# Optimization experiments

Measured on AMD Instinct MI355X. Metric: run time of the kernel, lower is better.

## Reference

```python
import jax, jax.numpy as jnp
import numpy as np

D_MODEL = 1024
N_HEADS = 16
CHUNK = 64
EPS = 1e-6


def elu_plus_1(x):
    return jax.nn.elu(x) + 1.0


def setup_inputs() -> dict:
    key = jax.random.key(0)
    kx, kq, kk, kv, ko = jax.random.split(key, 5)
    B, T = 4, 4096
    # xavier_uniform for square (D, D) weights: limit = sqrt(6/(D+D))
    lim = float(np.sqrt(6.0 / (D_MODEL + D_MODEL)))
    mk = lambda k: jax.random.uniform(k, (D_MODEL, D_MODEL), jnp.float32, -lim, lim)
    return {
        "x": jax.random.normal(kx, (B, T, D_MODEL), jnp.float32),
        "W_q": mk(kq),
        "W_k": mk(kk),
        "W_v": mk(kv),
        "W_o": mk(ko),
    }


def reference(x, W_q, W_k, W_v, W_o):
    B, T, D = x.shape
    H = N_HEADS
    dk = D // H
    dv = dk
    C = CHUNK
    N = T // C  # T chosen divisible by chunk size (no padding needed)

    q = (x @ W_q.T).reshape(B, T, H, dk)
    k = (x @ W_k.T).reshape(B, T, H, dk)
    v = (x @ W_v.T).reshape(B, T, H, dv)

    phi_q = elu_plus_1(q).reshape(B, N, C, H, dk)
    phi_k = elu_plus_1(k).reshape(B, N, C, H, dk)
    vc = v.reshape(B, N, C, H, dv)

    # Per-chunk key-value outer products and key sums, then exclusive prefix
    # sums over chunks give the carried state S and normalizer z at each
    # chunk's start (same math as the sequential chunk loop).
    KV = jnp.einsum('bnchk,bnchv->bnhkv', phi_k, vc)      # (B,N,H,dk,dv)
    Ksum = phi_k.sum(axis=2)                               # (B,N,C->sum,H,dk) -> (B,N,H,dk)
    KV_cum = jnp.cumsum(KV, axis=1)
    Ksum_cum = jnp.cumsum(Ksum, axis=1)
    S_prefix = jnp.concatenate([jnp.zeros_like(KV_cum[:, :1]), KV_cum[:, :-1]], axis=1)
    z_prefix = jnp.concatenate([jnp.zeros_like(Ksum_cum[:, :1]), Ksum_cum[:, :-1]], axis=1)

    # Inter-chunk contribution from carried state
    inter = jnp.einsum('bnchk,bnhkv->bnchv', phi_q, S_prefix)   # (B,N,C,H,dv)
    z_inter = jnp.einsum('bnchk,bnhk->bnch', phi_q, z_prefix)   # (B,N,C,H)

    # Intra-chunk causal attention
    mask = jnp.tril(jnp.ones((C, C), dtype=x.dtype))
    attn = jnp.einsum('bnihk,bnjhk->bnhij', phi_q, phi_k) * mask  # (B,N,H,C,C)
    intra = jnp.einsum('bnhij,bnjhv->bnihv', attn, vc)            # (B,N,C,H,dv)
    z_intra = attn.sum(axis=-1).transpose(0, 1, 3, 2)             # (B,N,C,H)

    denom = jnp.clip((z_inter + z_intra)[..., None], 1e-6, None)
    y = (inter + intra) / denom                                   # (B,N,C,H,dv)
    y = y.reshape(B, T, H * dv)
    return y @ W_o.T
```

## Files before the change

kernel.cpp:

```cpp
#include <hip/hip_runtime.h>


typedef unsigned short u16;
typedef float  f32x4 __attribute__((ext_vector_type(4)));
typedef short  b16x8 __attribute__((ext_vector_type(8)));
typedef u16    u16x4 __attribute__((ext_vector_type(4)));
typedef u16    u16x8 __attribute__((ext_vector_type(8)));

#define DEVINL __device__ __forceinline__

DEVINL u16 f2b(float f) {
  unsigned u = __float_as_uint(f);
  return (u16)((u + 0x7fffu + ((u >> 16) & 1u)) >> 16);
}
DEVINL float b2f(u16 s) { return __uint_as_float(((unsigned)s) << 16); }

DEVINL f32x4 mfma16(b16x8 a, b16x8 b, f32x4 c) {
  return __builtin_amdgcn_mfma_f32_16x16x32_bf16(a, b, c, 0, 0, 0);
}

DEVINL float phi_elu1(float v) { return v > 0.f ? v + 1.f : __expf(v); }

__global__ void cvt_kernel(const float* __restrict__ in, u16* __restrict__ out, int n8) {
  int stride = gridDim.x * blockDim.x;
  for (int i = blockIdx.x * blockDim.x + threadIdx.x; i < n8; i += stride) {
    const float* p = in + (size_t)i * 8;
    f32x4 a = *(const f32x4*)p;
    f32x4 b = *(const f32x4*)(p + 4);
    u16x8 o;
    o[0] = f2b(a[0]); o[1] = f2b(a[1]); o[2] = f2b(a[2]); o[3] = f2b(a[3]);
    o[4] = f2b(b[0]); o[5] = f2b(b[1]); o[6] = f2b(b[2]); o[7] = f2b(b[3]);
    *(u16x8*)(out + (size_t)i * 8) = o;
  }
}

__global__ void cvt4_kernel(const float* __restrict__ p0, const float* __restrict__ p1,
                            const float* __restrict__ p2, const float* __restrict__ p3,
                            u16* __restrict__ o0, u16* __restrict__ o1,
                            u16* __restrict__ o2, u16* __restrict__ o3) {
  const float* in; u16* out;
  switch (blockIdx.y) {
    case 0: in = p0; out = o0; break;
    case 1: in = p1; out = o1; break;
    case 2: in = p2; out = o2; break;
    default: in = p3; out = o3; break;
  }
  int i = blockIdx.x * blockDim.x + threadIdx.x;
  const float* p = in + (size_t)i * 8;
  f32x4 a = *(const f32x4*)p;
  f32x4 b = *(const f32x4*)(p + 4);
  u16x8 o;
  o[0] = f2b(a[0]); o[1] = f2b(a[1]); o[2] = f2b(a[2]); o[3] = f2b(a[3]);
  o[4] = f2b(b[0]); o[5] = f2b(b[1]); o[6] = f2b(b[2]); o[7] = f2b(b[3]);
  *(u16x8*)(out + (size_t)i * 8) = o;
}

#define GEMM_SETUP                                                              \
  __shared__ char lds[131072];                                                  \
  const int tid = threadIdx.x, wid = tid >> 6, l = tid & 63;                    \
  const int l15 = l & 15, lg = l >> 4;                                          \
  const int wr = wid >> 2, wc = wid & 3;                                        \
  const int ntn = N >> 8;                                                       \
  const int nwg = gridDim.x, bid = blockIdx.x;                                  \
  const int cpx = nwg >> 3;                                                     \
  const int sb = (bid & 7) * cpx + (bid >> 3);                                  \
  const int tm = sb / ntn, tn = sb - tm * ntn;                                  \
  const int colX0 = (lg * 16) ^ ((l15 & 7) << 4);                               \
  const int colX1 = (64 + lg * 16) ^ ((l15 & 7) << 4);                          \
  char* ldsA = lds + wr * 16384 + l15 * 128;                                    \
  char* ldsB = lds + 32768 + (wc >> 1) * 16384 + ((wc & 1) * 64 + l15) * 128;   \
  const int srow = tid >> 3;                                                    \
  const int scol = ((((tid & 7) * 16) ^ ((srow & 7) << 4)) >> 1);               \
  const u16* sA = A + (size_t)(tm * 256 + srow) * 1024 + scol;                  \
  const u16* sB = B + (size_t)(tn * 256 + srow) * 1024 + scol;                  \
  char* ldsStage = lds + wid * 1024;

#define STAGE(tt, h)                                                            \
  do {                                                                          \
    const u16* s_ = ((h) < 2 ? sA : sB) + (size_t)(((h) & 1) * 128) * 1024 +    \
                    (size_t)(tt) * 64;                                          \
    char* d_ = ldsStage + (((tt) & 1) << 16) + ((h) < 2 ? 0 : 32768) +          \
               (((h) & 1) << 14);                                               \
    __builtin_amdgcn_global_load_lds(                                           \
        (const __attribute__((address_space(1))) void*)(s_),                    \
        (__attribute__((address_space(3))) void*)(d_), 16, 0, 0);               \
    __builtin_amdgcn_global_load_lds(                                           \
        (const __attribute__((address_space(1))) void*)(s_ + 64 * 1024),        \
        (__attribute__((address_space(3))) void*)(d_ + 8192), 16, 0, 0);        \
  } while (0)

#define BAR_SB()                                                                \
  do {                                                                          \
    __builtin_amdgcn_s_barrier();                                               \
    __builtin_amdgcn_sched_barrier(0);                                          \
  } while (0)

#define GEMM_EPILOGUE                                                           \
  _Pragma("unroll") for (int fm = 0; fm < 8; ++fm)                              \
    _Pragma("unroll") for (int fn = 0; fn < 4; ++fn)                            \
      _Pragma("unroll") for (int r = 0; r < 4; ++r) {                           \
        size_t grow = (size_t)tm * 256 + wr * 128 + fm * 16 + lg * 4 + r;       \
        size_t gcol = (size_t)tn * 256 + wc * 64 + fn * 16 + l15;               \
        float v = acc[fm][fn][r];                                               \
        if (PHI) v = phi_elu1(v);                                               \
        OT* p = C + grow * (size_t)N + gcol;                                    \
        if constexpr (sizeof(OT) == 2) *p = (OT)f2b(v);                         \
        else                           *p = (OT)v;                              \
      }

template <bool PHI, typename OT>
__global__ __launch_bounds__(512, 2) void gemm256f(const u16* __restrict__ A,
                                                   const u16* __restrict__ B,
                                                   OT* __restrict__ C, int M, int N) {
  GEMM_SETUP

  f32x4 acc[8][4];
#pragma unroll
  for (int i = 0; i < 8; i++)
#pragma unroll
    for (int j = 0; j < 4; j++) acc[i][j] = f32x4{0.f, 0.f, 0.f, 0.f};

  STAGE(0, 0); STAGE(0, 1); STAGE(0, 2); STAGE(0, 3);
  STAGE(1, 2); STAGE(1, 3);
  asm volatile("s_waitcnt vmcnt(4)" ::: "memory");

  b16x8 a0[4], a1[4], b0[4], b1[4];
  for (int t = 0; t < 16; ++t) {
    const int cb = (t & 1) << 16;
    BAR_SB();
#pragma unroll
    for (int fm = 0; fm < 4; fm++) a0[fm] = *(const b16x8*)(ldsA + cb + fm * 2048 + colX0);
#pragma unroll
    for (int fn = 0; fn < 4; fn++) b0[fn] = *(const b16x8*)(ldsB + cb + fn * 2048 + colX0);
    if (t < 15) STAGE(t + 1, 0);
    __builtin_amdgcn_s_setprio(1);
#pragma unroll
    for (int fm = 0; fm < 4; fm++)
#pragma unroll
      for (int fn = 0; fn < 4; fn++) acc[fm][fn] = mfma16(a0[fm], b0[fn], acc[fm][fn]);
    __builtin_amdgcn_s_setprio(0);
    BAR_SB();
#pragma unroll
    for (int fm = 0; fm < 4; fm++) a1[fm] = *(const b16x8*)(ldsA + cb + (4 + fm) * 2048 + colX0);
#pragma unroll
    for (int fn = 0; fn < 4; fn++) b1[fn] = *(const b16x8*)(ldsB + cb + fn * 2048 + colX1);
    if (t < 15) STAGE(t + 1, 1);
    __builtin_amdgcn_s_setprio(1);
#pragma unroll
    for (int fm = 0; fm < 4; fm++)
#pragma unroll
      for (int fn = 0; fn < 4; fn++) acc[4 + fm][fn] = mfma16(a1[fm], b0[fn], acc[4 + fm][fn]);
    __builtin_amdgcn_s_setprio(0);
    BAR_SB();
#pragma unroll
    for (int fm = 0; fm < 4; fm++) a0[fm] = *(const b16x8*)(ldsA + cb + fm * 2048 + colX1);
    if (t < 14) STAGE(t + 2, 2);
    __builtin_amdgcn_s_setprio(1);
#pragma unroll
    for (int fm = 0; fm < 4; fm++)
#pragma unroll
      for (int fn = 0; fn < 4; fn++) acc[fm][fn] = mfma16(a0[fm], b1[fn], acc[fm][fn]);
    __builtin_amdgcn_s_setprio(0);
    BAR_SB();
#pragma unroll
    for (int fm = 0; fm < 4; fm++) a1[fm] = *(const b16x8*)(ldsA + cb + (4 + fm) * 2048 + colX1);
    if (t < 14) STAGE(t + 2, 3);
    __builtin_amdgcn_s_setprio(1);
#pragma unroll
    for (int fm = 0; fm < 4; fm++)
#pragma unroll
      for (int fn = 0; fn < 4; fn++) acc[4 + fm][fn] = mfma16(a1[fm], b1[fn], acc[4 + fm][fn]);
    __builtin_amdgcn_s_setprio(0);
    if (t < 14) asm volatile("s_waitcnt vmcnt(4)" ::: "memory");
    else        asm volatile("s_waitcnt vmcnt(0)" ::: "memory");
  }

  GEMM_EPILOGUE
}

template <bool PHI, typename OT>
__global__ __launch_bounds__(512, 2) void gemm256g(const u16* __restrict__ A,
                                                   const u16* __restrict__ B,
                                                   OT* __restrict__ C, int M, int N) {
  GEMM_SETUP

  f32x4 acc[8][4];
#pragma unroll
  for (int i = 0; i < 8; i++)
#pragma unroll
    for (int j = 0; j < 4; j++) acc[i][j] = f32x4{0.f, 0.f, 0.f, 0.f};

  STAGE(0, 0); STAGE(0, 1); STAGE(0, 2); STAGE(0, 3);
  STAGE(1, 2); STAGE(1, 3);
  asm volatile("s_waitcnt vmcnt(4)" ::: "memory");

  b16x8 a0[4], a1[4], b0[4], b1[4];
  for (int t = 0; t < 16; ++t) {
    const int cb = (t & 1) << 16;
    BAR_SB();
#pragma unroll
    for (int fm = 0; fm < 4; fm++) {
      a0[fm] = *(const b16x8*)(ldsA + cb + fm * 2048 + colX0);
      a1[fm] = *(const b16x8*)(ldsA + cb + (4 + fm) * 2048 + colX0);
    }
#pragma unroll
    for (int fn = 0; fn < 4; fn++) b0[fn] = *(const b16x8*)(ldsB + cb + fn * 2048 + colX0);
    if (t < 15) { STAGE(t + 1, 0); STAGE(t + 1, 1); }
    __builtin_amdgcn_s_setprio(1);
#pragma unroll
    for (int fm = 0; fm < 4; fm++)
#pragma unroll
      for (int fn = 0; fn < 4; fn++) acc[fm][fn] = mfma16(a0[fm], b0[fn], acc[fm][fn]);
#pragma unroll
    for (int fm = 0; fm < 4; fm++)
#pragma unroll
      for (int fn = 0; fn < 4; fn++) acc[4 + fm][fn] = mfma16(a1[fm], b0[fn], acc[4 + fm][fn]);
    __builtin_amdgcn_s_setprio(0);
    BAR_SB();
#pragma unroll
    for (int fm = 0; fm < 4; fm++) {
      a0[fm] = *(const b16x8*)(ldsA + cb + fm * 2048 + colX1);
      a1[fm] = *(const b16x8*)(ldsA + cb + (4 + fm) * 2048 + colX1);
    }
#pragma unroll
    for (int fn = 0; fn < 4; fn++) b1[fn] = *(const b16x8*)(ldsB + cb + fn * 2048 + colX1);
    if (t < 14) { STAGE(t + 2, 2); STAGE(t + 2, 3); }
    __builtin_amdgcn_s_setprio(1);
#pragma unroll
    for (int fm = 0; fm < 4; fm++)
#pragma unroll
      for (int fn = 0; fn < 4; fn++) acc[fm][fn] = mfma16(a0[fm], b1[fn], acc[fm][fn]);
#pragma unroll
    for (int fm = 0; fm < 4; fm++)
#pragma unroll
      for (int fn = 0; fn < 4; fn++) acc[4 + fm][fn] = mfma16(a1[fm], b1[fn], acc[4 + fm][fn]);
    __builtin_amdgcn_s_setprio(0);
    if (t < 14) asm volatile("s_waitcnt vmcnt(4)" ::: "memory");
    else        asm volatile("s_waitcnt vmcnt(0)" ::: "memory");
  }

  GEMM_EPILOGUE
}

__global__ __launch_bounds__(256) void transpose64(const u16* __restrict__ in,
                                                   u16* __restrict__ out) {
  __shared__ u16 tile[64][68];
  const int t = threadIdx.x;
  const int tr = blockIdx.x, tc = blockIdx.y;
#pragma unroll
  for (int i = 0; i < 4; i++) {
    int idx = i * 256 + t, r = idx >> 4, c4 = idx & 15;
    u16x4 v = *(const u16x4*)(in + (size_t)(tr * 64 + r) * 1024 + tc * 64 + c4 * 4);
    *(u16x4*)&tile[r][c4 * 4] = v;
  }
  __syncthreads();
#pragma unroll
  for (int i = 0; i < 4; i++) {
    int idx = i * 256 + t, oc = idx >> 4, r4 = idx & 15;
    u16x4 v;
    v[0] = tile[r4 * 4 + 0][oc]; v[1] = tile[r4 * 4 + 1][oc];
    v[2] = tile[r4 * 4 + 2][oc]; v[3] = tile[r4 * 4 + 3][oc];
    *(u16x4*)(out + (size_t)(tc * 64 + oc) * 16384 + tr * 64 + r4 * 4) = v;
  }
}

__global__ __launch_bounds__(256, 2) void kv_kernel(const u16* __restrict__ kT,
                                                    const u16* __restrict__ vT,
                                                    u16* __restrict__ KVT,
                                                    float* __restrict__ Ksum) {
  const int tid = threadIdx.x, wid = tid >> 6, l = tid & 63, l15 = l & 15, lg = l >> 4;
  const int bid = blockIdx.x, hg = bid & 3, bn = bid >> 2, n = bn & 63, b = bn >> 6;
  const int h = hg * 4 + wid;
  const size_t cb = (size_t)b * 4096 + n * 64 + lg * 8;

  b16x8 af[4][2], bf[4][2];
#pragma unroll
  for (int fm = 0; fm < 4; fm++)
#pragma unroll
    for (int ks = 0; ks < 2; ks++)
      af[fm][ks] = *(const b16x8*)(vT + (size_t)(h * 64 + fm * 16 + l15) * 16384 + cb + ks * 32);
#pragma unroll
  for (int fn = 0; fn < 4; fn++)
#pragma unroll
    for (int ks = 0; ks < 2; ks++)
      bf[fn][ks] = *(const b16x8*)(kT + (size_t)(h * 64 + fn * 16 + l15) * 16384 + cb + ks * 32);

  f32x4 acc[4][4];
#pragma unroll
  for (int i = 0; i < 4; i++)
#pragma unroll
    for (int j = 0; j < 4; j++) acc[i][j] = f32x4{0.f, 0.f, 0.f, 0.f};
#pragma unroll
  for (int ks = 0; ks < 2; ks++)
#pragma unroll
    for (int fm = 0; fm < 4; fm++)
#pragma unroll
      for (int fn = 0; fn < 4; fn++) acc[fm][fn] = mfma16(af[fm][ks], bf[fn][ks], acc[fm][fn]);

  float ksum[4] = {0.f, 0.f, 0.f, 0.f};
#pragma unroll
  for (int fn = 0; fn < 4; fn++) {
#pragma unroll
    for (int ks = 0; ks < 2; ks++)
#pragma unroll
      for (int j = 0; j < 8; j++) ksum[fn] += b2f((u16)bf[fn][ks][j]);
    ksum[fn] += __shfl_xor(ksum[fn], 16);
    ksum[fn] += __shfl_xor(ksum[fn], 32);
  }
  const size_t ob = (size_t)(b * 16 + h) * 64 + n;
  if (l < 16) {
#pragma unroll
    for (int fn = 0; fn < 4; fn++) Ksum[ob * 64 + fn * 16 + l15] = ksum[fn];
  }
#pragma unroll
  for (int fm = 0; fm < 4; fm++)
#pragma unroll
    for (int fn = 0; fn < 4; fn++)
#pragma unroll
      for (int r = 0; r < 4; r++)
        KVT[ob * 4096 + (size_t)(fm * 16 + lg * 4 + r) * 64 + fn * 16 + l15] =
            f2b(acc[fm][fn][r]);
}

__global__ __launch_bounds__(256) void scan_s(const u16* __restrict__ KVT,
                                              u16* __restrict__ ST,
                                              const float* __restrict__ Ksum,
                                              float* __restrict__ zpre) {
  if (blockIdx.x >= 1024) {
    const int gi = (blockIdx.x - 1024) * 256 + threadIdx.x;
    const size_t bh = gi >> 6;
    const int dk = gi & 63;
    float acc = 0.f;
    for (int n = 0; n < 64; n++) {
      size_t idx = (bh * 64 + n) * 64 + dk;
      zpre[idx] = acc;
      acc += Ksum[idx];
    }
    return;
  }
  const size_t base = (size_t)(blockIdx.x >> 4) * 64 * 4096 +
                      (blockIdx.x & 15) * 256 + threadIdx.x;
  float acc = 0.f;
  float v[4], w[4];
#pragma unroll
  for (int i = 0; i < 4; i++) v[i] = b2f(KVT[base + (size_t)i * 4096]);
  for (int n = 0; n < 64; n += 4) {
    if (n < 60) {
#pragma unroll
      for (int i = 0; i < 4; i++) w[i] = b2f(KVT[base + (size_t)(n + 4 + i) * 4096]);
    } else {
#pragma unroll
      for (int i = 0; i < 4; i++) w[i] = 0.f;
    }
#pragma unroll
    for (int i = 0; i < 4; i++) {
      ST[base + (size_t)(n + i) * 4096] = f2b(acc);
      acc += v[i];
    }
#pragma unroll
    for (int i = 0; i < 4; i++) v[i] = w[i];
  }
}

__global__ __launch_bounds__(256, 2) void attn_out(const u16* __restrict__ phiQ,
                                                   const u16* __restrict__ phiK,
                                                   const u16* __restrict__ vT,
                                                   const u16* __restrict__ ST,
                                                   const float* __restrict__ zpre,
                                                   u16* __restrict__ Y) {
  __shared__ char lds[4 * 8192 + 4 * 256];
  const int tid = threadIdx.x, wid = tid >> 6, l = tid & 63, l15 = l & 15, lg = l >> 4;
  const int bid = blockIdx.x, hg = bid & 3, bn = bid >> 2, n = bn & 63, b = bn >> 6;
  const int h = hg * 4 + wid;
  const size_t row0 = (size_t)b * 4096 + n * 64;
  const int dcol = h * 64;

  b16x8 qf[4][2];
#pragma unroll
  for (int fi = 0; fi < 4; fi++)
#pragma unroll
    for (int ks = 0; ks < 2; ks++)
      qf[fi][ks] = *(const b16x8*)(phiQ + (row0 + fi * 16 + l15) * 1024 + dcol + lg * 8 + ks * 32);

  f32x4 accT[4][4];
#pragma unroll
  for (int i = 0; i < 4; i++)
#pragma unroll
    for (int j = 0; j < 4; j++) accT[i][j] = f32x4{0.f, 0.f, 0.f, 0.f};
  {
    b16x8 kf[4][2];
#pragma unroll
    for (int fj = 0; fj < 4; fj++)
#pragma unroll
      for (int ks = 0; ks < 2; ks++)
        kf[fj][ks] = *(const b16x8*)(phiK + (row0 + fj * 16 + l15) * 1024 + dcol + lg * 8 + ks * 32);
#pragma unroll
    for (int ks = 0; ks < 2; ks++)
#pragma unroll
      for (int fj = 0; fj < 4; fj++)
#pragma unroll
        for (int fi = 0; fi < 4; fi++)
          accT[fj][fi] = mfma16(kf[fj][ks], qf[fi][ks], accT[fj][fi]);
  }

  const size_t zb = ((size_t)(b * 16 + h) * 64 + n) * 64;
  float zi[4] = {0.f, 0.f, 0.f, 0.f};
#pragma unroll
  for (int ks = 0; ks < 2; ks++) {
    f32x4 z0 = *(const f32x4*)(zpre + zb + lg * 8 + ks * 32);
    f32x4 z1 = *(const f32x4*)(zpre + zb + lg * 8 + ks * 32 + 4);
#pragma unroll
    for (int fi = 0; fi < 4; fi++)
#pragma unroll
      for (int j = 0; j < 4; j++) {
        zi[fi] += b2f((u16)qf[fi][ks][j])     * z0[j];
        zi[fi] += b2f((u16)qf[fi][ks][j + 4]) * z1[j];
      }
  }

  char* abuf = lds + wid * 8192;
  float zt[4] = {0.f, 0.f, 0.f, 0.f};
#pragma unroll
  for (int fi = 0; fi < 4; fi++) {
    const int i = fi * 16 + l15;
    const int swz = (i & 7) << 4;
#pragma unroll
    for (int fj = 0; fj < 4; fj++) {
      f32x4 v = accT[fj][fi];
#pragma unroll
      for (int r = 0; r < 4; r++) {
        int j = fj * 16 + lg * 4 + r;
        if (j > i) v[r] = 0.f;
        zt[fi] += v[r];
      }
      unsigned w0 = (unsigned)f2b(v[0]) | ((unsigned)f2b(v[1]) << 16);
      unsigned w1 = (unsigned)f2b(v[2]) | ((unsigned)f2b(v[3]) << 16);
      int jb = (fj * 16 + lg * 4) * 2;
      *(unsigned*)(abuf + i * 128 + (jb ^ swz)) = w0;
      *(unsigned*)(abuf + i * 128 + ((jb + 4) ^ swz)) = w1;
    }
  }

  float* dbuf = (float*)(lds + 32768 + wid * 256);
#pragma unroll
  for (int fi = 0; fi < 4; fi++) {
    float z = zi[fi] + zt[fi];
    z += __shfl_xor(z, 16);
    z += __shfl_xor(z, 32);
    float rd = 1.f / fmaxf(z, 1e-6f);
    if (l < 16) dbuf[fi * 16 + l15] = rd;
  }
  __syncthreads();

  b16x8 stf[4][2], vf[4][2];
  const size_t stb = ((size_t)(b * 16 + h) * 64 + n) * 4096;
#pragma unroll
  for (int fn = 0; fn < 4; fn++)
#pragma unroll
    for (int ks = 0; ks < 2; ks++) {
      stf[fn][ks] = *(const b16x8*)(ST + stb + (size_t)(fn * 16 + l15) * 64 + lg * 8 + ks * 32);
      vf[fn][ks]  = *(const b16x8*)(vT + (size_t)(dcol + fn * 16 + l15) * 16384 +
                                    (size_t)b * 4096 + n * 64 + lg * 8 + ks * 32);
    }
  f32x4 acc[4][4];
#pragma unroll
  for (int i = 0; i < 4; i++)
#pragma unroll
    for (int j = 0; j < 4; j++) acc[i][j] = f32x4{0.f, 0.f, 0.f, 0.f};
#pragma unroll
  for (int ks = 0; ks < 2; ks++)
#pragma unroll
    for (int fm = 0; fm < 4; fm++)
#pragma unroll
      for (int fn = 0; fn < 4; fn++) acc[fm][fn] = mfma16(qf[fm][ks], stf[fn][ks], acc[fm][fn]);
#pragma unroll
  for (int fm = 0; fm < 4; fm++) {
    const int i = fm * 16 + l15;
    const int swz = (i & 7) << 4;
#pragma unroll
    for (int ks = 0; ks < 2; ks++) {
      b16x8 af = *(const b16x8*)(abuf + i * 128 + ((ks * 64 + lg * 16) ^ swz));
#pragma unroll
      for (int fn = 0; fn < 4; fn++) acc[fm][fn] = mfma16(af, vf[fn][ks], acc[fm][fn]);
    }
  }

#pragma unroll
  for (int fm = 0; fm < 4; fm++)
#pragma unroll
    for (int r = 0; r < 4; r++) {
      float rd = dbuf[fm * 16 + lg * 4 + r];
#pragma unroll
      for (int fn = 0; fn < 4; fn++)
        Y[(row0 + fm * 16 + lg * 4 + r) * 1024 + dcol + fn * 16 + l15] =
            f2b(acc[fm][fn][r] * rd);
    }
}

extern "C" void kernel_launch(void* const* d_in, const int* in_sizes, int n_in,
                              void* d_out, int out_size, void* d_ws, size_t ws_size,
                              hipStream_t stream) {
  const float* x  = (const float*)d_in[0];
  const float* Wq = (const float*)d_in[1];
  const float* Wk = (const float*)d_in[2];
  const float* Wv = (const float*)d_in[3];
  const float* Wo = (const float*)d_in[4];
  float* out = (float*)d_out;

  char* ws = (char*)d_ws;
  size_t off = 0;
  auto alloc = [&](size_t bytes) -> char* {
    char* p = ws + off;
    off += (bytes + 255) & ~(size_t)255;
    return p;
  };
  u16*   xb   = (u16*)alloc(33554432);
  u16*   wqb  = (u16*)alloc(2097152);
  u16*   wkb  = (u16*)alloc(2097152);
  u16*   wvb  = (u16*)alloc(2097152);
  u16*   wob  = (u16*)alloc(2097152);
  u16*   phiQ = (u16*)alloc(33554432);
  u16*   phiK = (u16*)alloc(33554432);
  u16*   vT   = (u16*)alloc(33554432);
  u16*   kT   = (u16*)alloc(33554432);
  u16*   KVT  = (u16*)alloc(33554432);
  float* Ksum = (float*)alloc(1048576);
  u16*   ST   = (u16*)alloc(33554432);
  float* zpre = (float*)alloc(1048576);
  u16*   y    = xb;

  cvt_kernel<<<2048, 256, 0, stream>>>(x, xb, 2097152);
  cvt4_kernel<<<dim3(512, 4), 256, 0, stream>>>(Wq, Wk, Wv, Wo, wqb, wkb, wvb, wob);

  gemm256g<true, u16><<<256, 512, 0, stream>>>(xb, wqb, phiQ, 16384, 1024);
  gemm256f<true, u16><<<256, 512, 0, stream>>>(xb, wkb, phiK, 16384, 1024);
  gemm256f<false, u16><<<256, 512, 0, stream>>>(wvb, xb, vT, 1024, 16384);

  transpose64<<<dim3(256, 16), 256, 0, stream>>>(phiK, kT);
  kv_kernel<<<1024, 256, 0, stream>>>(kT, vT, KVT, Ksum);
  scan_s<<<1040, 256, 0, stream>>>(KVT, ST, Ksum, zpre);
  attn_out<<<1024, 256, 0, stream>>>(phiQ, phiK, vT, ST, zpre, y);

  gemm256f<false, float><<<256, 512, 0, stream>>>(y, wob, out, 16384, 1024);
}
```

Baseline: 241.6 us.

## Fuse phiK transpose into kv_kernel via LDS and use gemm256g everywhere

Removes the standalone transpose64 kernel and the kT buffer. kv_kernel now loads phiK rows directly, stages them in shared memory, and reads transposed fragments from there. All GEMMs switch to the gemm256g schedule, which uses fewer barriers per k-step and issues larger batches of loads. This saves a full 32MB read plus write pass and one launch, at the cost of strided LDS reads in kv_kernel and higher register pressure in the GEMMs.

```diff
diff --git a/kernel.cpp b/kernel.cpp
--- a/kernel.cpp
+++ b/kernel.cpp
@@ -109,7 +109,7 @@
       }
 
 template <bool PHI, typename OT>
-__global__ __launch_bounds__(512, 2) void gemm256f(const u16* __restrict__ A,
+__global__ __launch_bounds__(512, 2) void gemm256g(const u16* __restrict__ A,
                                                    const u16* __restrict__ B,
                                                    OT* __restrict__ C, int M, int N) {
   GEMM_SETUP
@@ -129,23 +129,18 @@
     const int cb = (t & 1) << 16;
     BAR_SB();
 #pragma unroll
-    for (int fm = 0; fm < 4; fm++) a0[fm] = *(const b16x8*)(ldsA + cb + fm * 2048 + colX0);
+    for (int fm = 0; fm < 4; fm++) {
+      a0[fm] = *(const b16x8*)(ldsA + cb + fm * 2048 + colX0);
+      a1[fm] = *(const b16x8*)(ldsA + cb + (4 + fm) * 2048 + colX0);
+    }
 #pragma unroll
     for (int fn = 0; fn < 4; fn++) b0[fn] = *(const b16x8*)(ldsB + cb + fn * 2048 + colX0);
-    if (t < 15) STAGE(t + 1, 0);
+    if (t < 15) { STAGE(t + 1, 0); STAGE(t + 1, 1); }
     __builtin_amdgcn_s_setprio(1);
 #pragma unroll
     for (int fm = 0; fm < 4; fm++)
 #pragma unroll
       for (int fn = 0; fn < 4; fn++) acc[fm][fn] = mfma16(a0[fm], b0[fn], acc[fm][fn]);
-    __builtin_amdgcn_s_setprio(0);
-    BAR_SB();
-#pragma unroll
-    for (int fm = 0; fm < 4; fm++) a1[fm] = *(const b16x8*)(ldsA + cb + (4 + fm) * 2048 + colX0);
-#pragma unroll
-    for (int fn = 0; fn < 4; fn++) b1[fn] = *(const b16x8*)(ldsB + cb + fn * 2048 + colX1);
-    if (t < 15) STAGE(t + 1, 1);
-    __builtin_amdgcn_s_setprio(1);
 #pragma unroll
     for (int fm = 0; fm < 4; fm++)
 #pragma unroll
@@ -153,19 +148,18 @@
     __builtin_amdgcn_s_setprio(0);
     BAR_SB();
 #pragma unroll
-    for (int fm = 0; fm < 4; fm++) a0[fm] = *(const b16x8*)(ldsA + cb + fm * 2048 + colX1);
-    if (t < 14) STAGE(t + 2, 2);
+    for (int fm = 0; fm < 4; fm++) {
+      a0[fm] = *(const b16x8*)(ldsA + cb + fm * 2048 + colX1);
+      a1[fm] = *(const b16x8*)(ldsA + cb + (4 + fm) * 2048 + colX1);
+    }
+#pragma unroll
+    for (int fn = 0; fn < 4; fn++) b1[fn] = *(const b16x8*)(ldsB + cb + fn * 2048 + colX1);
+    if (t < 14) { STAGE(t + 2, 2); STAGE(t + 2, 3); }
     __builtin_amdgcn_s_setprio(1);
 #pragma unroll
     for (int fm = 0; fm < 4; fm++)
 #pragma unroll
       for (int fn = 0; fn < 4; fn++) acc[fm][fn] = mfma16(a0[fm], b1[fn], acc[fm][fn]);
-    __builtin_amdgcn_s_setprio(0);
-    BAR_SB();
-#pragma unroll
-    for (int fm = 0; fm < 4; fm++) a1[fm] = *(const b16x8*)(ldsA + cb + (4 + fm) * 2048 + colX1);
-    if (t < 14) STAGE(t + 2, 3);
-    __builtin_amdgcn_s_setprio(1);
 #pragma unroll
     for (int fm = 0; fm < 4; fm++)
 #pragma unroll
@@ -178,112 +172,47 @@
   GEMM_EPILOGUE
 }
 
-template <bool PHI, typename OT>
-__global__ __launch_bounds__(512, 2) void gemm256g(const u16* __restrict__ A,
-                                                   const u16* __restrict__ B,
-                                                   OT* __restrict__ C, int M, int N) {
-  GEMM_SETUP
-
-  f32x4 acc[8][4];
-#pragma unroll
-  for (int i = 0; i < 8; i++)
-#pragma unroll
-    for (int j = 0; j < 4; j++) acc[i][j] = f32x4{0.f, 0.f, 0.f, 0.f};
-
-  STAGE(0, 0); STAGE(0, 1); STAGE(0, 2); STAGE(0, 3);
-  STAGE(1, 2); STAGE(1, 3);
-  asm volatile("s_waitcnt vmcnt(4)" ::: "memory");
-
-  b16x8 a0[4], a1[4], b0[4], b1[4];
-  for (int t = 0; t < 16; ++t) {
-    const int cb = (t & 1) << 16;
-    BAR_SB();
-#pragma unroll
-    for (int fm = 0; fm < 4; fm++) {
-      a0[fm] = *(const b16x8*)(ldsA + cb + fm * 2048 + colX0);
-      a1[fm] = *(const b16x8*)(ldsA + cb + (4 + fm) * 2048 + colX0);
-    }
-#pragma unroll
-    for (int fn = 0; fn < 4; fn++) b0[fn] = *(const b16x8*)(ldsB + cb + fn * 2048 + colX0);
-    if (t < 15) { STAGE(t + 1, 0); STAGE(t + 1, 1); }
-    __builtin_amdgcn_s_setprio(1);
-#pragma unroll
-    for (int fm = 0; fm < 4; fm++)
-#pragma unroll
-      for (int fn = 0; fn < 4; fn++) acc[fm][fn] = mfma16(a0[fm], b0[fn], acc[fm][fn]);
-#pragma unroll
-    for (int fm = 0; fm < 4; fm++)
-#pragma unroll
-      for (int fn = 0; fn < 4; fn++) acc[4 + fm][fn] = mfma16(a1[fm], b0[fn], acc[4 + fm][fn]);
-    __builtin_amdgcn_s_setprio(0);
-    BAR_SB();
-#pragma unroll
-    for (int fm = 0; fm < 4; fm++) {
-      a0[fm] = *(const b16x8*)(ldsA + cb + fm * 2048 + colX1);
-      a1[fm] = *(const b16x8*)(ldsA + cb + (4 + fm) * 2048 + colX1);
-    }
-#pragma unroll
-    for (int fn = 0; fn < 4; fn++) b1[fn] = *(const b16x8*)(ldsB + cb + fn * 2048 + colX1);
-    if (t < 14) { STAGE(t + 2, 2); STAGE(t + 2, 3); }
-    __builtin_amdgcn_s_setprio(1);
-#pragma unroll
-    for (int fm = 0; fm < 4; fm++)
-#pragma unroll
-      for (int fn = 0; fn < 4; fn++) acc[fm][fn] = mfma16(a0[fm], b1[fn], acc[fm][fn]);
-#pragma unroll
-    for (int fm = 0; fm < 4; fm++)
-#pragma unroll
-      for (int fn = 0; fn < 4; fn++) acc[4 + fm][fn] = mfma16(a1[fm], b1[fn], acc[4 + fm][fn]);
-    __builtin_amdgcn_s_setprio(0);
-    if (t < 14) asm volatile("s_waitcnt vmcnt(4)" ::: "memory");
-    else        asm volatile("s_waitcnt vmcnt(0)" ::: "memory");
-  }
-
-  GEMM_EPILOGUE
-}
-
-__global__ __launch_bounds__(256) void transpose64(const u16* __restrict__ in,
-                                                   u16* __restrict__ out) {
-  __shared__ u16 tile[64][68];
-  const int t = threadIdx.x;
-  const int tr = blockIdx.x, tc = blockIdx.y;
-#pragma unroll
-  for (int i = 0; i < 4; i++) {
-    int idx = i * 256 + t, r = idx >> 4, c4 = idx & 15;
-    u16x4 v = *(const u16x4*)(in + (size_t)(tr * 64 + r) * 1024 + tc * 64 + c4 * 4);
-    *(u16x4*)&tile[r][c4 * 4] = v;
-  }
-  __syncthreads();
-#pragma unroll
-  for (int i = 0; i < 4; i++) {
-    int idx = i * 256 + t, oc = idx >> 4, r4 = idx & 15;
-    u16x4 v;
-    v[0] = tile[r4 * 4 + 0][oc]; v[1] = tile[r4 * 4 + 1][oc];
-    v[2] = tile[r4 * 4 + 2][oc]; v[3] = tile[r4 * 4 + 3][oc];
-    *(u16x4*)(out + (size_t)(tc * 64 + oc) * 16384 + tr * 64 + r4 * 4) = v;
-  }
-}
-
-__global__ __launch_bounds__(256, 2) void kv_kernel(const u16* __restrict__ kT,
+__global__ __launch_bounds__(256, 2) void kv_kernel(const u16* __restrict__ phiK,
                                                     const u16* __restrict__ vT,
                                                     u16* __restrict__ KVT,
                                                     float* __restrict__ Ksum) {
+  __shared__ u16 tile[4][64][68];
   const int tid = threadIdx.x, wid = tid >> 6, l = tid & 63, l15 = l & 15, lg = l >> 4;
   const int bid = blockIdx.x, hg = bid & 3, bn = bid >> 2, n = bn & 63, b = bn >> 6;
   const int h = hg * 4 + wid;
+  const size_t row0 = (size_t)b * 4096 + n * 64;
+  const int dcol = h * 64;
   const size_t cb = (size_t)b * 4096 + n * 64 + lg * 8;
 
-  b16x8 af[4][2], bf[4][2];
+  b16x8 af[4][2];
 #pragma unroll
   for (int fm = 0; fm < 4; fm++)
 #pragma unroll
     for (int ks = 0; ks < 2; ks++)
       af[fm][ks] = *(const b16x8*)(vT + (size_t)(h * 64 + fm * 16 + l15) * 16384 + cb + ks * 32);
+
+  u16 (*tw)[68] = tile[wid];
+#pragma unroll
+  for (int i = 0; i < 8; i++) {
+    int tok = i * 8 + (l >> 3);
+    int c8 = (l & 7) * 8;
+    u16x8 v = *(const u16x8*)(phiK + (row0 + tok) * 1024 + dcol + c8);
+    *(u16x4*)(&tw[tok][c8]) = u16x4{v[0], v[1], v[2], v[3]};
+    *(u16x4*)(&tw[tok][c8 + 4]) = u16x4{v[4], v[5], v[6], v[7]};
+  }
+  __syncthreads();
+
+  b16x8 bf[4][2];
 #pragma unroll
   for (int fn = 0; fn < 4; fn++)
 #pragma unroll
-    for (int ks = 0; ks < 2; ks++)
-      bf[fn][ks] = *(const b16x8*)(kT + (size_t)(h * 64 + fn * 16 + l15) * 16384 + cb + ks * 32);
+    for (int ks = 0; ks < 2; ks++) {
+      b16x8 t;
+#pragma unroll
+      for (int j = 0; j < 8; j++)
+        t[j] = (short)tw[lg * 8 + ks * 32 + j][fn * 16 + l15];
+      bf[fn][ks] = t;
+    }
 
   f32x4 acc[4][4];
 #pragma unroll
@@ -522,7 +451,6 @@
   u16*   phiQ = (u16*)alloc(33554432);
   u16*   phiK = (u16*)alloc(33554432);
   u16*   vT   = (u16*)alloc(33554432);
-  u16*   kT   = (u16*)alloc(33554432);
   u16*   KVT  = (u16*)alloc(33554432);
   float* Ksum = (float*)alloc(1048576);
   u16*   ST   = (u16*)alloc(33554432);
@@ -533,13 +461,12 @@
   cvt4_kernel<<<dim3(512, 4), 256, 0, stream>>>(Wq, Wk, Wv, Wo, wqb, wkb, wvb, wob);
 
   gemm256g<true, u16><<<256, 512, 0, stream>>>(xb, wqb, phiQ, 16384, 1024);
-  gemm256f<true, u16><<<256, 512, 0, stream>>>(xb, wkb, phiK, 16384, 1024);
-  gemm256f<false, u16><<<256, 512, 0, stream>>>(wvb, xb, vT, 1024, 16384);
-
-  transpose64<<<dim3(256, 16), 256, 0, stream>>>(phiK, kT);
-  kv_kernel<<<1024, 256, 0, stream>>>(kT, vT, KVT, Ksum);
+  gemm256g<true, u16><<<256, 512, 0, stream>>>(xb, wkb, phiK, 16384, 1024);
+  gemm256g<false, u16><<<256, 512, 0, stream>>>(wvb, xb, vT, 1024, 16384);
+
+  kv_kernel<<<1024, 256, 0, stream>>>(phiK, vT, KVT, Ksum);
   scan_s<<<1040, 256, 0, stream>>>(KVT, ST, Ksum, zpre);
   attn_out<<<1024, 256, 0, stream>>>(phiQ, phiK, vT, ST, zpre, y);
 
-  gemm256f<false, float><<<256, 512, 0, stream>>>(y, wob, out, 16384, 1024);
-}
+  gemm256g<false, float><<<256, 512, 0, stream>>>(y, wob, out, 16384, 1024);
+}
```

Measured after the change: 233.1 us. -3.5%, faster.
